# Kernel optimization log

Hardware: AMD Instinct MI355X
Metric: run time of the kernel (lower is better)

## Reference

```python
import jax, jax.numpy as jnp
import numpy as np

N_CHANNELS = 512
D_K = 64
N_HEADS = N_CHANNELS // D_K  # 8
SCALE = 1.0 / np.sqrt(np.sqrt(D_K))
EPS = 1e-8


def pixnorm(x, axis=-1):
    return x * jax.lax.rsqrt(jnp.mean(x * x, axis=axis, keepdims=True) + EPS)


def setup_inputs() -> dict:
    key = jax.random.key(0)
    k1, k2, k3 = jax.random.split(key, 3)
    x = jax.random.normal(k1, (16, N_CHANNELS, 32, 32), dtype=jnp.float32)
    # 1x1 conv weights (bias=False) stored as [out, in]
    w_proj = jax.random.normal(k2, (3 * N_CHANNELS, N_CHANNELS), dtype=jnp.float32) * (1.0 / np.sqrt(N_CHANNELS))
    w_out = jax.random.normal(k3, (N_CHANNELS, N_CHANNELS), dtype=jnp.float32) * (1.0 / np.sqrt(N_CHANNELS))
    return {"x": x, "w_proj": w_proj, "w_out": w_out}


def reference(x, w_proj, w_out):
    B, C, H, W = x.shape
    S = H * W
    # tokens: [B, S, C]
    xt = x.reshape(B, C, S).transpose(0, 2, 1)
    # 1x1 conv projection -> [B, S, 3C]
    h = jnp.einsum('bsc,oc->bso', xt, w_proj)
    qkv = h.reshape(B, S, N_HEADS, 3 * D_K)
    q, k, v = jnp.split(qkv, 3, axis=-1)  # each [B, S, H, d]
    q = pixnorm(q)
    k = pixnorm(k)
    v = pixnorm(v)
    attn = jnp.einsum('bihd,bjhd->bijh', q * SCALE, k * SCALE)
    attn = jax.nn.softmax(attn, axis=2)
    res = jnp.einsum('bijh,bjhd->bihd', attn, v)  # [B, S, H, d]
    res = res.reshape(B, S, C)
    res = jnp.einsum('bsc,oc->bso', res, w_out)
    res = res.transpose(0, 2, 1).reshape(B, C, H, W)
    return x + res
```

## Files before the change

kernel.cpp:

```cpp
#include <hip/hip_runtime.h>
#include <hip/hip_bf16.h>
#include <math.h>

typedef float f32x4 __attribute__((ext_vector_type(4)));
typedef __bf16 bf16x8 __attribute__((ext_vector_type(8)));
typedef __bf16 bf16x4 __attribute__((ext_vector_type(4)));
typedef unsigned u32x4 __attribute__((ext_vector_type(4)));

#define DEVFN static __device__ __forceinline__

DEVFN void gload16(const void* g, void* l) {
  __builtin_amdgcn_global_load_lds(
      (const __attribute__((address_space(1))) unsigned int*)g,
      (__attribute__((address_space(3))) unsigned int*)l, 16, 0, 0);
}

DEVFN f32x4 mfma16(bf16x8 a, bf16x8 b, f32x4 c) {
  return __builtin_amdgcn_mfma_f32_16x16x32_bf16(a, b, c, 0, 0, 0);
}

DEVFN unsigned cvtpk(float lo, float hi) {
  unsigned r;
  asm("v_cvt_pk_bf16_f32 %0, %1, %2" : "=v"(r) : "v"(lo), "v"(hi));
  return r;
}

#define WAITV4() asm volatile("s_waitcnt vmcnt(4)" ::: "memory")
#define WAITV0() asm volatile("s_waitcnt vmcnt(0)" ::: "memory")

__global__ __launch_bounds__(256) void transpose_x_k(
    const float* __restrict__ x, __bf16* __restrict__ xt,
    const float* __restrict__ wp, const float* __restrict__ wo,
    __bf16* __restrict__ wpb, __bf16* __restrict__ wob) {
  __shared__ float tile[64][65];
  int b = blockIdx.z, c0 = blockIdx.y * 64, s0 = blockIdx.x * 64;
  int t = threadIdx.x;
  int r = t >> 2, q = (t & 3) << 4;
  const float* src = x + ((size_t)(b * 512 + c0 + r)) * 1024 + s0 + q;
#pragma unroll
  for (int i = 0; i < 4; i++) {
    float4 f = *reinterpret_cast<const float4*>(src + i * 4);
    tile[r][q + i * 4 + 0] = f.x;
    tile[r][q + i * 4 + 1] = f.y;
    tile[r][q + i * 4 + 2] = f.z;
    tile[r][q + i * 4 + 3] = f.w;
  }
  int lid = (blockIdx.z * 8 + blockIdx.y) * 16 + blockIdx.x;
  int wi = lid * 512 + t * 2;
  if (wi < 786432) {
    float2 f = *reinterpret_cast<const float2*>(wp + wi);
    wpb[wi] = (__bf16)f.x;
    wpb[wi + 1] = (__bf16)f.y;
  } else {
    int j = wi - 786432;
    float2 f = *reinterpret_cast<const float2*>(wo + j);
    wob[j] = (__bf16)f.x;
    wob[j + 1] = (__bf16)f.y;
  }
  __syncthreads();
  bf16x8 o0, o1;
#pragma unroll
  for (int i = 0; i < 8; i++) o0[i] = (__bf16)tile[q + i][r];
#pragma unroll
  for (int i = 0; i < 8; i++) o1[i] = (__bf16)tile[q + 8 + i][r];
  __bf16* dst = xt + ((size_t)(b * 1024 + s0 + r)) * 512 + c0 + q;
  *reinterpret_cast<bf16x8*>(dst) = o0;
  *reinterpret_cast<bf16x8*>(dst + 8) = o1;
}

template <int MODE>
__global__ __launch_bounds__(256, 4) void gemm_bt_k(
    const __bf16* __restrict__ A, const __bf16* __restrict__ Bt,
    float* __restrict__ Cf, const float* __restrict__ Xres,
    __bf16* __restrict__ Qo, __bf16* __restrict__ Ko, __bf16* __restrict__ Vto) {
  __shared__ __attribute__((aligned(16))) char smem[49152];
  int p = blockIdx.x, xcd = p & 7, idx = p >> 3;
  int m0, n0, z;
  if (MODE == 2) {
    m0 = (xcd * 16 + idx / 12) * 128;
    n0 = (idx % 12) * 128;
    z = 0;
  } else {
    z = xcd * 2 + idx / 32;
    int rem = idx % 32;
    m0 = (rem >> 3) * 128;
    n0 = (rem & 7) * 128;
    Bt += (size_t)z * (1024L * 512);
  }
  int tid = threadIdx.x, wave = tid >> 6, lane = tid & 63;
  int fr = lane & 15, fq = lane >> 4;
  int wm = (wave >> 1) * 64, wn = (wave & 1) * 64;
  f32x4 acc[4][4] = {};
  int offs[2], rr[2], scc[2];
#pragma unroll
  for (int i = 0; i < 2; i++) {
    offs[i] = wave * 2048 + i * 1024 + lane * 16;
    rr[i] = offs[i] >> 6;
    scc[i] = (offs[i] & 63) ^ (((rr[i] ^ (rr[i] >> 2)) & 3) << 4);
  }
  int rdsw = (fr ^ (fr >> 2)) & 3;
  const char* Ap = (const char*)A;
  const char* Bp = (const char*)Bt;

#define GSTAGE(k0_, slot_)                                                      \
  {                                                                             \
    char* as_ = smem + (slot_)*16384;                                           \
    char* bs_ = as_ + 8192;                                                     \
    _Pragma("unroll") for (int i = 0; i < 2; i++)                               \
        gload16(Ap + (size_t)(m0 + rr[i]) * 1024 + (k0_)*2 + scc[i],            \
                as_ + offs[i]);                                                 \
    _Pragma("unroll") for (int i = 0; i < 2; i++)                               \
        gload16(Bp + (size_t)(n0 + rr[i]) * 1024 + (k0_)*2 + scc[i],            \
                bs_ + offs[i]);                                                 \
  }

  GSTAGE(0, 0);
  GSTAGE(32, 1);
#pragma unroll
  for (int t = 0; t < 16; t++) {
    if (t < 15) WAITV4(); else WAITV0();
    __builtin_amdgcn_s_barrier();
    __builtin_amdgcn_sched_barrier(0);
    const char* as = smem + (t % 3) * 16384;
    const char* bs = as + 8192;
    bf16x8 af[4], bfr[4];
#pragma unroll
    for (int mi = 0; mi < 4; mi++)
      af[mi] = *reinterpret_cast<const bf16x8*>(
          as + (wm + mi * 16 + fr) * 64 + ((fq ^ rdsw) << 4));
#pragma unroll
    for (int ni = 0; ni < 4; ni++)
      bfr[ni] = *reinterpret_cast<const bf16x8*>(
          bs + (wn + ni * 16 + fr) * 64 + ((fq ^ rdsw) << 4));
    if (t + 2 < 16) GSTAGE((t + 2) * 32, (t + 2) % 3);
    __builtin_amdgcn_s_setprio(1);
#pragma unroll
    for (int mi = 0; mi < 4; mi++)
#pragma unroll
      for (int ni = 0; ni < 4; ni++)
        acc[mi][ni] = mfma16(af[mi], bfr[ni], acc[mi][ni]);
    __builtin_amdgcn_s_setprio(0);
  }
#undef GSTAGE

  if (MODE == 1) {
    float* Co = Cf + (size_t)z * (512L * 1024);
    const float* Xr = Xres + (size_t)z * (512L * 1024);
#pragma unroll
    for (int mi = 0; mi < 4; mi++)
#pragma unroll
      for (int i = 0; i < 4; i++) {
        int row = m0 + wm + mi * 16 + fq * 4 + i;
#pragma unroll
        for (int ni = 0; ni < 4; ni++) {
          size_t idxo = (size_t)row * 1024 + n0 + wn + ni * 16 + fr;
          Co[idxo] = acc[mi][ni][i] + Xr[idxo];
        }
      }
  } else {
    int g0 = n0 + wn;
    int head = g0 / 192;
    int grp = (g0 >> 6) % 3;
    int b = m0 >> 10, sb = m0 & 1023;
    int bh = b * 8 + head;
    float nrm[4][4];
#pragma unroll
    for (int mi = 0; mi < 4; mi++)
#pragma unroll
      for (int i = 0; i < 4; i++) {
        float ss = 0.f;
#pragma unroll
        for (int ni = 0; ni < 4; ni++) ss += acc[mi][ni][i] * acc[mi][ni][i];
#pragma unroll
        for (int off = 1; off < 16; off <<= 1) ss += __shfl_xor(ss, off);
        float nv = rsqrtf(ss * (1.0f / 64.0f) + 1e-8f);
        if (grp == 0) nv *= 0.18033688011112042f;
        nrm[mi][i] = nv;
      }
    if (grp < 2) {
      __bf16* dst = (grp == 0 ? Qo : Ko) + (size_t)bh * 65536;
#pragma unroll
      for (int mi = 0; mi < 4; mi++)
#pragma unroll
        for (int i = 0; i < 4; i++) {
          int s = sb + wm + mi * 16 + fq * 4 + i;
#pragma unroll
          for (int ni = 0; ni < 4; ni++)
            dst[(size_t)s * 64 + ni * 16 + fr] = (__bf16)(acc[mi][ni][i] * nrm[mi][i]);
        }
    }
    __syncthreads();
    if (grp == 2) {
#pragma unroll
      for (int mi = 0; mi < 4; mi++)
#pragma unroll
        for (int i = 0; i < 4; i++) {
          int r = wm + mi * 16 + fq * 4 + i;
#pragma unroll
          for (int ni = 0; ni < 4; ni++) {
            int col2 = (2 * (ni * 16 + fr)) ^ ((r & 31) << 2);
            *(__bf16*)(smem + r * 128 + col2) = (__bf16)(acc[mi][ni][i] * nrm[mi][i]);
          }
        }
    }
    __syncthreads();
    if (grp == 2) {
      int sl = wm + lane;
      int l = sl & 63;
      int pl = ((l >> 2) & 3) * 16 + (l >> 4) * 4 + (l & 3);
      __bf16* vdst = Vto + (size_t)bh * 65536 + sb + (sl & 64) + pl;
#pragma unroll 8
      for (int d = 0; d < 64; d++) {
        __bf16 v = *(const __bf16*)(smem + sl * 128 + ((2 * d) ^ ((sl & 31) << 2)));
        vdst[(size_t)d * 1024] = v;
      }
    }
  }
}

__global__ __launch_bounds__(256, 2) void attn_k(const __bf16* __restrict__ Q,
                                                 const __bf16* __restrict__ Kb,
                                                 const __bf16* __restrict__ Vt,
                                                 __bf16* __restrict__ Res) {
  __shared__ __attribute__((aligned(16))) char lds[49152];
  int p = blockIdx.x;
  int v = (p & 7) * 64 + (p >> 3);
  int qt = v & 3, bh = v >> 2;
  int wave = threadIdx.x >> 6, lane = threadIdx.x & 63;
  int fr = lane & 15, fq = lane >> 4;
  const __bf16* Qb = Q + (size_t)bh * 65536;
  const char* Kbase = (const char*)(Kb + (size_t)bh * 65536);
  const char* Vbase = (const char*)(Vt + (size_t)bh * 65536);
  bf16x8 qf[4][2];
#pragma unroll
  for (int qs = 0; qs < 4; qs++)
#pragma unroll
    for (int kk = 0; kk < 2; kk++)
      qf[qs][kk] = *reinterpret_cast<const bf16x8*>(
          Qb + (size_t)(qt * 256 + qs * 64 + wave * 16 + fr) * 64 + kk * 32 + fq * 8);

  bf16x8 ones;
#pragma unroll
  for (int j = 0; j < 8; j++) ones[j] = (__bf16)1.0f;

  f32x4 oa[4][4] = {};
  f32x4 lacc[4] = {};

  int o0 = wave * 2048 + lane * 16;
  int o1 = o0 + 1024;
  int r0 = o0 >> 7, c0 = o0 & 127, r1 = o1 >> 7, c1 = o1 & 127;
  int s0 = c0 ^ ((r0 & 7) << 4), s1 = c1 ^ ((r1 & 7) << 4);
  int swr = (fr & 7) << 4;

#define STAGE(kt_, slot_)                                                       \
  {                                                                             \
    char* ks_ = lds + (slot_)*16384;                                            \
    char* vs_ = ks_ + 8192;                                                     \
    gload16(Kbase + (size_t)(kt_)*8192 + r0 * 128 + s0, ks_ + o0);              \
    gload16(Kbase + (size_t)(kt_)*8192 + r1 * 128 + s1, ks_ + o1);              \
    gload16(Vbase + (size_t)r0 * 2048 + (kt_)*128 + s0, vs_ + o0);              \
    gload16(Vbase + (size_t)r1 * 2048 + (kt_)*128 + s1, vs_ + o1);              \
  }

  STAGE(0, 0);
  STAGE(1, 1);
  for (int kt = 0; kt < 16; kt++) {
    if (kt < 15) WAITV4(); else WAITV0();
    __builtin_amdgcn_s_barrier();
    __builtin_amdgcn_sched_barrier(0);
    if (kt + 2 < 16) STAGE(kt + 2, (kt + 2) % 3);
    const char* ksc = lds + (kt % 3) * 16384;
    const char* vsc = ksc + 8192;
    f32x4 sa[4][4] = {};
    __builtin_amdgcn_s_setprio(1);
#pragma unroll
    for (int ni = 0; ni < 4; ni++) {
      bf16x8 kf0 = *reinterpret_cast<const bf16x8*>(
          ksc + (ni * 16 + fr) * 128 + ((fq * 16) ^ swr));
      bf16x8 kf1 = *reinterpret_cast<const bf16x8*>(
          ksc + (ni * 16 + fr) * 128 + ((64 + fq * 16) ^ swr));
#pragma unroll
      for (int qs = 0; qs < 4; qs++) {
        sa[qs][ni] = mfma16(kf0, qf[qs][0], sa[qs][ni]);
        sa[qs][ni] = mfma16(kf1, qf[qs][1], sa[qs][ni]);
      }
    }
    __builtin_amdgcn_s_setprio(0);
    bf16x8 pb[4][2];
#pragma unroll
    for (int qs = 0; qs < 4; qs++) {
#pragma unroll
      for (int ni = 0; ni < 4; ni++)
#pragma unroll
        for (int i = 0; i < 4; i++)
          sa[qs][ni][i] = __builtin_amdgcn_exp2f(sa[qs][ni][i]);
#pragma unroll
      for (int kk2 = 0; kk2 < 2; kk2++) {
        u32x4 u;
        u[0] = cvtpk(sa[qs][2 * kk2][0], sa[qs][2 * kk2][1]);
        u[1] = cvtpk(sa[qs][2 * kk2][2], sa[qs][2 * kk2][3]);
        u[2] = cvtpk(sa[qs][2 * kk2 + 1][0], sa[qs][2 * kk2 + 1][1]);
        u[3] = cvtpk(sa[qs][2 * kk2 + 1][2], sa[qs][2 * kk2 + 1][3]);
        pb[qs][kk2] = __builtin_bit_cast(bf16x8, u);
      }
      lacc[qs] = mfma16(ones, pb[qs][0], lacc[qs]);
      lacc[qs] = mfma16(ones, pb[qs][1], lacc[qs]);
    }
    __builtin_amdgcn_s_setprio(1);
#pragma unroll
    for (int nd = 0; nd < 4; nd++) {
      int vrow = (nd * 16 + fr) * 128;
#pragma unroll
      for (int kk2 = 0; kk2 < 2; kk2++) {
        bf16x8 vf = *reinterpret_cast<const bf16x8*>(
            vsc + vrow + ((fq * 32 + kk2 * 16) ^ swr));
#pragma unroll
        for (int qs = 0; qs < 4; qs++)
          oa[qs][nd] = mfma16(vf, pb[qs][kk2], oa[qs][nd]);
      }
    }
    __builtin_amdgcn_s_setprio(0);
  }
  int b = bh >> 3, hd = bh & 7;
#pragma unroll
  for (int qs = 0; qs < 4; qs++) {
    int q = qt * 256 + qs * 64 + wave * 16 + fr;
    float inv_l = 1.0f / lacc[qs][0];
    __bf16* dst = Res + ((size_t)(b * 1024 + q)) * 512 + hd * 64 + fq * 4;
#pragma unroll
    for (int nd = 0; nd < 4; nd++) {
      bf16x4 ov;
#pragma unroll
      for (int i = 0; i < 4; i++) ov[i] = (__bf16)(oa[qs][nd][i] * inv_l);
      *reinterpret_cast<bf16x4*>(dst + nd * 16) = ov;
    }
  }
#undef STAGE
}

extern "C" void kernel_launch(void* const* d_in, const int* in_sizes, int n_in,
                              void* d_out, int out_size, void* d_ws, size_t ws_size,
                              hipStream_t stream) {
  const float* x = (const float*)d_in[0];
  const float* wp = (const float*)d_in[1];
  const float* wo = (const float*)d_in[2];
  float* out = (float*)d_out;
  char* w = (char*)d_ws;
  __bf16* wpb = (__bf16*)(w);
  __bf16* wob = (__bf16*)(w + 1572864);
  __bf16* xt = (__bf16*)(w + 2097152);
  __bf16* Qb = (__bf16*)(w + 18874368);
  __bf16* Kb = (__bf16*)(w + 35651584);
  __bf16* Vtb = (__bf16*)(w + 52428800);
  __bf16* resb = (__bf16*)(w + 69206016);

  transpose_x_k<<<dim3(16, 8, 16), 256, 0, stream>>>(x, xt, wp, wo, wpb, wob);
  gemm_bt_k<2><<<1536, 256, 0, stream>>>(xt, wpb, nullptr, nullptr, Qb, Kb, Vtb);
  attn_k<<<512, 256, 0, stream>>>(Qb, Kb, Vtb, resb);
  gemm_bt_k<1><<<512, 256, 0, stream>>>(wob, resb, out, x, nullptr, nullptr,
                                        nullptr);
}
```

Baseline: 115.2 us.

## Add dedicated 512-thread output projection GEMM with swizzled double-buffered LDS

Replaces the generic templated GEMM for the output projection with a specialized kernel. It uses 512 threads per block on a 128x128 tile, a double-buffered LDS pipeline with a K-step of 32 fed by direct global-to-LDS loads, and XOR-swizzled LDS addressing. Blocks are mapped to XCDs so each XCD handles two batches. The aim is better latency hiding and L2 locality for the last GEMM, at the cost of more barriers per K step and a strided residual-add epilogue.

New measurement: 114.5 us (median of 3 runs). About the same (-0.6%).

```diff
diff --git a/kernel.cpp b/kernel.cpp
--- a/kernel.cpp
+++ b/kernel.cpp
@@ -26,6 +26,7 @@
 }
 
 #define WAITV4() asm volatile("s_waitcnt vmcnt(4)" ::: "memory")
+#define WAITV2() asm volatile("s_waitcnt vmcnt(2)" ::: "memory")
 #define WAITV0() asm volatile("s_waitcnt vmcnt(0)" ::: "memory")
 
 __global__ __launch_bounds__(256) void transpose_x_k(
@@ -218,6 +219,81 @@
   }
 }
 
+__global__ __launch_bounds__(512, 4) void gemm_out_k(
+    const __bf16* __restrict__ A, const __bf16* __restrict__ Bt,
+    float* __restrict__ Cf, const float* __restrict__ Xres) {
+  __shared__ __attribute__((aligned(16))) char smem[32768];
+  const int K = 512;
+  int p = blockIdx.x, xcd = p & 7, idx = p >> 3;
+  int z = xcd * 2 + idx / 32;
+  int rem = idx % 32;
+  int m0 = (rem >> 3) * 128;
+  int n0 = (rem & 7) * 128;
+  Bt += (size_t)z * (1024L * 512);
+  int tid = threadIdx.x, wave = tid >> 6, lane = tid & 63;
+  int fr = lane & 15, fq = lane >> 4;
+  int wm = (wave >> 2) * 64, wn = (wave & 3) * 32;
+  f32x4 acc[4][2] = {};
+  int offs = tid * 16;
+  int rr = offs >> 6;
+  int scc = (offs & 63) ^ (((rr ^ (rr >> 2)) & 3) << 4);
+  int rdsw = (fr ^ (fr >> 2)) & 3;
+  const char* Ap = (const char*)A;
+  const char* Bp = (const char*)Bt;
+
+#define GSTAGE2(k0_, slot_)                                                     \
+  {                                                                             \
+    char* as_ = smem + (slot_)*16384;                                           \
+    gload16(Ap + (size_t)(m0 + rr) * 1024 + (k0_)*2 + scc, as_ + offs);         \
+    gload16(Bp + (size_t)(n0 + rr) * 1024 + (k0_)*2 + scc, as_ + 8192 + offs);  \
+  }
+
+  GSTAGE2(0, 0);
+  GSTAGE2(32, 1);
+  int cur = 0;
+  for (int k0 = 0; k0 < K; k0 += 32) {
+    if (k0 + 32 < K) WAITV2(); else WAITV0();
+    __builtin_amdgcn_s_barrier();
+    __builtin_amdgcn_sched_barrier(0);
+    const char* as = smem + cur * 16384;
+    const char* bs = as + 8192;
+    bf16x8 af[4], bfr[2];
+#pragma unroll
+    for (int mi = 0; mi < 4; mi++)
+      af[mi] = *reinterpret_cast<const bf16x8*>(
+          as + (wm + mi * 16 + fr) * 64 + ((fq ^ rdsw) << 4));
+#pragma unroll
+    for (int ni = 0; ni < 2; ni++)
+      bfr[ni] = *reinterpret_cast<const bf16x8*>(
+          bs + (wn + ni * 16 + fr) * 64 + ((fq ^ rdsw) << 4));
+    __builtin_amdgcn_s_setprio(1);
+#pragma unroll
+    for (int mi = 0; mi < 4; mi++)
+#pragma unroll
+      for (int ni = 0; ni < 2; ni++)
+        acc[mi][ni] = mfma16(af[mi], bfr[ni], acc[mi][ni]);
+    __builtin_amdgcn_s_setprio(0);
+    __builtin_amdgcn_s_barrier();
+    if (k0 + 64 < K) GSTAGE2(k0 + 64, cur);
+    cur ^= 1;
+  }
+#undef GSTAGE2
+
+  float* Co = Cf + (size_t)z * (512L * 1024);
+  const float* Xr = Xres + (size_t)z * (512L * 1024);
+#pragma unroll
+  for (int mi = 0; mi < 4; mi++)
+#pragma unroll
+    for (int i = 0; i < 4; i++) {
+      int row = m0 + wm + mi * 16 + fq * 4 + i;
+#pragma unroll
+      for (int ni = 0; ni < 2; ni++) {
+        size_t idxo = (size_t)row * 1024 + n0 + wn + ni * 16 + fr;
+        Co[idxo] = acc[mi][ni][i] + Xr[idxo];
+      }
+    }
+}
+
 __global__ __launch_bounds__(256, 2) void attn_k(const __bf16* __restrict__ Q,
                                                  const __bf16* __restrict__ Kb,
                                                  const __bf16* __restrict__ Vt,
@@ -357,6 +433,5 @@
   transpose_x_k<<<dim3(16, 8, 16), 256, 0, stream>>>(x, xt, wp, wo, wpb, wob);
   gemm_bt_k<2><<<1536, 256, 0, stream>>>(xt, wpb, nullptr, nullptr, Qb, Kb, Vtb);
   attn_k<<<512, 256, 0, stream>>>(Qb, Kb, Vtb, resb);
-  gemm_bt_k<1><<<512, 256, 0, stream>>>(wob, resb, out, x, nullptr, nullptr,
-                                        nullptr);
-}
+  gemm_out_k<<<512, 512, 0, stream>>>(wob, resb, out, x);
+}
```
